# Kernel optimization log

Measured on AMD Instinct MI355X. Metric: run time of the kernel, lower is better.

## Reference

```python
import jax, jax.numpy as jnp
import numpy as np
import math

B, D = 8192, 128
STEEPNESS = 1.0
TOPK_NEG = 10
N_SORT = TOPK_NEG + 1  # n_pos_augs - 1 + topk_neg = 1 + 10
EPS = 1e-8


def setup_inputs() -> dict:
    key = jax.random.key(0)
    k1, k2 = jax.random.split(key)
    aug1 = jax.random.normal(k1, (B, D), dtype=jnp.float32)
    aug2 = jax.random.normal(k2, (B, D), dtype=jnp.float32)
    return {"aug1": aug1, "aug2": aug2}


def _soft_sort_odd_even(x, steepness):
    """Differentiable odd-even transposition sort (diffsort, cauchy interpolation).
    x: [B, n]. Returns (sorted_x [B, n], P [B, n, n]) where sorted_x = x @ P and
    P[i, j] = relaxed probability that input element i lands at sorted position j."""
    b, n = x.shape
    P = jnp.broadcast_to(jnp.eye(n, dtype=x.dtype), (b, n, n))
    for layer in range(n):  # n layers, alternating even/odd pairs
        off = layer % 2
        idx_a = np.arange(off, n - 1, 2)
        idx_b = idx_a + 1
        a = x[:, idx_a]
        bb = x[:, idx_b]
        # cauchy CDF relaxation: alpha -> 1 when b > a (already ordered)
        alpha = jnp.arctan(steepness * (bb - a)) / math.pi + 0.5
        x = x.at[:, idx_a].set(alpha * a + (1.0 - alpha) * bb)
        x = x.at[:, idx_b].set((1.0 - alpha) * a + alpha * bb)
        Pa = P[:, :, idx_a]
        Pb = P[:, :, idx_b]
        al = alpha[:, None, :]
        P = P.at[:, :, idx_a].set(al * Pa + (1.0 - al) * Pb)
        P = P.at[:, :, idx_b].set((1.0 - al) * Pa + al * Pb)
    return x, P


def _bce(p, t):
    # torch.nn.BCELoss with log clamped at -100
    logp = jnp.clip(jnp.log(p), -100.0, None)
    log1mp = jnp.clip(jnp.log(1.0 - p), -100.0, None)
    return -jnp.mean(t * logp + (1.0 - t) * log1mp)


def _compute_loss(anchor, positive):
    anchor = anchor.astype(jnp.float32)
    positive = jax.lax.stop_gradient(positive.astype(jnp.float32))  # stop_grad=True
    # pairwise cosine similarity (dim=1)
    an = anchor / jnp.maximum(jnp.linalg.norm(anchor, axis=1, keepdims=True), EPS)
    pn = positive / jnp.maximum(jnp.linalg.norm(positive, axis=1, keepdims=True), EPS)
    pos_sims = jnp.sum(an * pn, axis=1, keepdims=True)  # [B, 1]; sort over dim=1 is a no-op
    # all-to-all cosine similarity vs detached anchors (negatives = anchor.detach())
    negs = jax.lax.stop_gradient(an)
    sim = an @ negs.T  # [B, B]
    nb = sim.shape[0]
    sim = jnp.where(jnp.eye(nb, dtype=bool), -jnp.inf, sim)  # mask self-similarity
    neg_top, _ = jax.lax.top_k(sim, TOPK_NEG)  # descending
    neg_top = neg_top[:, ::-1]                 # flip -> ascending
    sims = jnp.concatenate([neg_top, pos_sims], axis=1)  # [B, 11]
    _, P = _soft_sort_odd_even(sims, STEEPNESS)
    n = sims.shape[1]
    # perm_target = identity -> column-sum targets are first-k indicators
    p_neg = jnp.clip(jnp.sum(P[:, :, :TOPK_NEG], axis=2), 0.0, 1.0)  # [B, n]
    p_pos = jnp.clip(jnp.sum(P[:, :, TOPK_NEG:], axis=2), 0.0, 1.0)
    t_neg = jnp.broadcast_to((jnp.arange(n) < TOPK_NEG).astype(jnp.float32), (nb, n))
    t_pos = 1.0 - t_neg
    return 0.5 * (_bce(p_pos, t_pos) + _bce(p_neg, t_neg))


def reference(aug1, aug2):
    # n_augs = 2: each aug serves as anchor once, the other as the single positive
    loss1 = _compute_loss(aug1, aug2)
    loss2 = _compute_loss(aug2, aug1)
    return (loss1 + loss2) / 2.0
```

## Files before the change

kernel.cpp:

```cpp
#include <hip/hip_runtime.h>
#include <cstdint>
#include <cmath>

#define NB 8192
#define ND 128
#define CAP 64
#define NEG_INF (-__builtin_inff())

typedef __attribute__((ext_vector_type(8))) __bf16 bf16x8;
typedef __attribute__((ext_vector_type(2))) __bf16 bf16x2;
typedef __attribute__((ext_vector_type(4))) float f32x4;


__device__ __forceinline__ void insert10(float t[10], float v) {
#pragma unroll
  for (int j = 0; j < 9; ++j) t[j] = __builtin_amdgcn_fmed3f(t[j], t[j + 1], v);
  t[9] = fmaxf(t[9], v);
}
__device__ __forceinline__ void insert11(float t[11], float v) {
#pragma unroll
  for (int j = 0; j < 10; ++j) t[j] = __builtin_amdgcn_fmed3f(t[j], t[j + 1], v);
  t[10] = fmaxf(t[10], v);
}

__device__ float row_loss(float x[11]) {
  float al[55];
#pragma unroll
  for (int layer = 0; layer < 11; ++layer) {
#pragma unroll
    for (int p = 0; p < 5; ++p) {
      int ii = (layer & 1) + 2 * p;
      float av = x[ii], bv = x[ii + 1];
      float a = atanf(bv - av) * 0.3183098861837907f + 0.5f;
      al[layer * 5 + p] = a;
      float be = 1.f - a;
      x[ii] = a * av + be * bv;
      x[ii + 1] = be * av + a * bv;
    }
  }
  float v[11];
#pragma unroll
  for (int i = 0; i < 11; ++i) v[i] = 0.f;
  v[10] = 1.f;
#pragma unroll
  for (int layer = 10; layer >= 0; --layer) {
#pragma unroll
    for (int p = 0; p < 5; ++p) {
      int ii = (layer & 1) + 2 * p;
      float a = al[layer * 5 + p];
      float be = 1.f - a;
      float va = v[ii], vb = v[ii + 1];
      v[ii] = a * va + be * vb;
      v[ii + 1] = be * va + a * vb;
    }
  }
  float C = fmaxf(logf(v[10]), -100.f);
#pragma unroll
  for (int i = 0; i < 10; ++i) C += fmaxf(logf(1.f - v[i]), -100.f);
  return C;
}

__global__ __launch_bounds__(256, 4) void knorm(const float* __restrict__ aug1,
                                                const float* __restrict__ aug2,
                                                __bf16* __restrict__ an,
                                                float* __restrict__ pos,
                                                float* __restrict__ out) {
  if (blockIdx.x == 0 && threadIdx.x == 0) out[0] = 0.f;
  int wid = threadIdx.x >> 6;
  int l = threadIdx.x & 63;
  int row = blockIdx.x * 4 + wid;
  const float2* a1 = (const float2*)(aug1) + (size_t)row * 64;
  const float2* a2 = (const float2*)(aug2) + (size_t)row * 64;
  float2 v1 = a1[l], v2 = a2[l];
  float ss1 = v1.x * v1.x + v1.y * v1.y;
  float ss2 = v2.x * v2.x + v2.y * v2.y;
  float dp = v1.x * v2.x + v1.y * v2.y;
#pragma unroll
  for (int off = 1; off < 64; off <<= 1) {
    ss1 += __shfl_xor(ss1, off);
    ss2 += __shfl_xor(ss2, off);
    dp += __shfl_xor(dp, off);
  }
  float inv1 = 1.0f / fmaxf(sqrtf(ss1), 1e-8f);
  float inv2 = 1.0f / fmaxf(sqrtf(ss2), 1e-8f);
  bf16x2 o1, o2;
  o1[0] = (__bf16)(v1.x * inv1);
  o1[1] = (__bf16)(v1.y * inv1);
  o2[0] = (__bf16)(v2.x * inv2);
  o2[1] = (__bf16)(v2.y * inv2);
  int unit = ((row >> 4) << 8) + ((l >> 4) << 6) + (((l >> 2) & 3) << 4) + (row & 15);
  ((bf16x2*)(an))[unit * 4 + (l & 3)] = o1;
  ((bf16x2*)(an + (size_t)NB * ND))[unit * 4 + (l & 3)] = o2;
  if (l == 0) pos[row] = dp * inv1 * inv2;
}

__device__ __forceinline__ void consume4(const f32x4* acc, float (*cand)[CAP],
                                         int* lcnt, float tau, int c) {
#pragma unroll
  for (int rb = 0; rb < 4; ++rb) {
    int rl = rb * 16 + c;
#pragma unroll
    for (int r = 0; r < 4; ++r) {
      float v = acc[rb][r];
      if (v > tau) {
        int s = atomicAdd(&lcnt[rl], 1);
        if (s < CAP) cand[rl][s] = v;
      }
    }
  }
}

__global__ __launch_bounds__(256, 3) void kgram(const __bf16* __restrict__ an_all,
                                                float* __restrict__ tk,
                                                int* __restrict__ cnth,
                                                float* __restrict__ taug) {
  int dir = blockIdx.y;
  int rowg = blockIdx.x >> 1;
  int half = blockIdx.x & 1;
  const bf16x8* an8 = (const bf16x8*)(an_all + (size_t)dir * NB * ND);
  int w = threadIdx.x >> 6;
  int l = threadIdx.x & 63;
  int q = l >> 4;
  int c = l & 15;
  int row_base = rowg * 64;
  const int col0 = half * 4096;

  __shared__ float cand[64][CAP];
  __shared__ int lcnt[64];
  __shared__ float sred[2][4];
  if (threadIdx.x < 64) lcnt[threadIdx.x] = 0;

  bf16x8 brow[4][4];
#pragma unroll
  for (int rb = 0; rb < 4; ++rb)
#pragma unroll
    for (int kc = 0; kc < 4; ++kc)
      brow[rb][kc] = an8[(size_t)row_base * 16 + rb * 256 + kc * 64 + l];

  const bf16x8* pf0 = an8 + ((size_t)col0 * 16 + w * 256 + l);
  bf16x8 a[4], a2[4];
  const f32x4 zz = {0.f, 0.f, 0.f, 0.f};
  f32x4 accA[4], accB[4];

  auto loadA = [&](int t) {
    const bf16x8* p = pf0 + (size_t)(t & 63) * 1024;
#pragma unroll
    for (int kc = 0; kc < 4; ++kc) a[kc] = p[kc * 64];
  };
  auto loadA2 = [&](int t) {
    const bf16x8* p = pf0 + (size_t)(t & 63) * 1024;
#pragma unroll
    for (int kc = 0; kc < 4; ++kc) a2[kc] = p[kc * 64];
  };
  auto mfma_tile = [&](f32x4* A, const bf16x8* src) {
#pragma unroll
    for (int rb = 0; rb < 4; ++rb)
      A[rb] = __builtin_amdgcn_mfma_f32_16x16x32_bf16(src[0], brow[rb][0], zz, 0, 0, 0);
#pragma unroll
    for (int kc = 1; kc < 4; ++kc)
#pragma unroll
      for (int rb = 0; rb < 4; ++rb)
        A[rb] = __builtin_amdgcn_mfma_f32_16x16x32_bf16(src[kc], brow[rb][kc], A[rb], 0, 0, 0);
  };

  loadA(0);
  mfma_tile(accA, a);
  loadA2(1);
  bool diag0 = (row_base == col0);
  int cq0 = col0 + w * 16 + q * 4;
  float s1 = 0.f, s2 = 0.f;
#pragma unroll
  for (int rb = 0; rb < 4; ++rb) {
    int myrow = row_base + rb * 16 + c;
#pragma unroll
    for (int r = 0; r < 4; ++r) {
      float v = accA[rb][r];
      v = (diag0 && (cq0 + r == myrow)) ? 0.f : v;
      s1 += v;
      s2 = fmaf(v, v, s2);
    }
  }
#pragma unroll
  for (int off = 1; off < 64; off <<= 1) {
    s1 += __shfl_xor(s1, off);
    s2 += __shfl_xor(s2, off);
  }
  if (l == 0) { sred[0][w] = s1; sred[1][w] = s2; }
  __syncthreads();
  float n = diag0 ? 4032.f : 4096.f;
  float ts1 = sred[0][0] + sred[0][1] + sred[0][2] + sred[0][3];
  float ts2 = sred[1][0] + sred[1][1] + sred[1][2] + sred[1][3];
  float mu = ts1 / n;
  float sig = sqrtf(fmaxf(ts2 / n - mu * mu, 0.f));
  float tau = mu + 2.5f * sig;
  if (threadIdx.x == 0) taug[(dir * 128 + rowg) * 2 + half] = tau;
  consume4(accA, cand, lcnt, tau, c);

  mfma_tile(accA, a2);
  loadA(2);
  for (int t = 2; t < 64; t += 2) {
    mfma_tile(accB, a);
    loadA2(t + 1);
    consume4(accA, cand, lcnt, tau, c);
    mfma_tile(accA, a2);
    loadA(t + 2);
    consume4(accB, cand, lcnt, tau, c);
  }
  consume4(accA, cand, lcnt, tau, c);

  __syncthreads();
  if (threadIdx.x < 64) {
    int rl = threadIdx.x;
    int cc = lcnt[rl];
    float t11[11];
#pragma unroll
    for (int j = 0; j < 11; ++j) t11[j] = NEG_INF;
    int m = cc < CAP ? cc : CAP;
    for (int i = 0; i < m; ++i) {
      float v = cand[rl][i];
      if (v > t11[0]) insert11(t11, v);
    }
    bool diagq = (row_base >= col0) && (row_base < col0 + 4096);
    float* o = tk + ((size_t)(dir * NB + row_base + rl) * 2 + half) * 10;
    if (diagq) {
#pragma unroll
      for (int j = 0; j < 10; ++j) o[j] = t11[j];
    } else {
#pragma unroll
      for (int j = 0; j < 10; ++j) o[j] = t11[j + 1];
    }
    cnth[(dir * NB + row_base + rl) * 2 + half] = cc;
  }
}

__global__ __launch_bounds__(64, 1) void ksort(const float* __restrict__ tk,
                                               const float* __restrict__ pos,
                                               const int* __restrict__ cnth,
                                               const float* __restrict__ taug,
                                               const __bf16* __restrict__ an_all,
                                               float* __restrict__ out) {
  int tid = blockIdx.x * 64 + threadIdx.x;
  int dir = tid >> 13;
  int row = tid & (NB - 1);
  int lane = threadIdx.x;

  const float* A = tk + (size_t)(dir * NB + row) * 20;
  float s10[10];
#pragma unroll
  for (int j = 0; j < 10; ++j) s10[j] = A[j];
#pragma unroll
  for (int j = 0; j < 10; ++j) {
    float v = A[10 + j];
    if (v > s10[0]) insert10(s10, v);
  }
  int rowg = row >> 6;
  float tmax = fmaxf(taug[(dir * 128 + rowg) * 2], taug[(dir * 128 + rowg) * 2 + 1]);
  int2 cc2 = ((const int2*)cnth)[dir * NB + row];
  bool ok = (cc2.x <= CAP) && (cc2.y <= CAP) && (s10[0] >= tmax);

  float C = 0.f;
  if (ok) {
    float x[11];
#pragma unroll
    for (int j = 0; j < 10; ++j) x[j] = s10[j];
    x[10] = pos[row];
    C = row_loss(x);
  }
#pragma unroll
  for (int off = 1; off < 64; off <<= 1) C += __shfl_xor(C, off);
  if (lane == 0) atomicAdd(out, C * (-1.f / (2.f * (float)NB * 11.f)));

  unsigned long long bad = __ballot(!ok);
  if (bad == 0ull) return;
  __shared__ float rv[128];
  __shared__ float lst[64][10];
  const __bf16* an = an_all + (size_t)dir * NB * ND;
  const bf16x8* an8 = (const bf16x8*)an;
  while (bad) {
    int b = __ffsll((long long)bad) - 1;
    bad &= bad - 1;
    int brow = (blockIdx.x * 64 + b) & (NB - 1);
    int u = ((brow >> 4) << 8) + ((lane >> 4) << 6) + (((lane >> 2) & 3) << 4) + (brow & 15);
    bf16x2 pr = ((const bf16x2*)an)[u * 4 + (lane & 3)];
    rv[lane * 2] = (float)pr[0];
    rv[lane * 2 + 1] = (float)pr[1];
    __syncthreads();
    float t10[10];
#pragma unroll
    for (int j = 0; j < 10; ++j) t10[j] = NEG_INF;
    for (int i = 0; i < 128; ++i) {
      int col = lane + i * 64;
      if (col == brow) continue;
      float d = 0.f;
#pragma unroll
      for (int j = 0; j < 16; ++j) {
        bf16x8 p = an8[(size_t)(col >> 4) * 256 + (j >> 2) * 64 + (j & 3) * 16 + (col & 15)];
        int kb = (j >> 2) * 32 + (j & 3) * 8;
#pragma unroll
        for (int e = 0; e < 8; ++e) d = fmaf(rv[kb + e], (float)p[e], d);
      }
      if (d > t10[0]) insert10(t10, d);
    }
#pragma unroll
    for (int j = 0; j < 10; ++j) lst[lane][j] = t10[j];
    __syncthreads();
    if (lane == 0) {
      float cur[10];
#pragma unroll
      for (int j = 0; j < 10; ++j) cur[j] = lst[0][j];
      for (int s = 1; s < 64; ++s)
        for (int j = 0; j < 10; ++j) {
          float v = lst[s][j];
          if (v > cur[0]) insert10(cur, v);
        }
      float x[11];
#pragma unroll
      for (int j = 0; j < 10; ++j) x[j] = cur[j];
      x[10] = pos[brow];
      atomicAdd(out, row_loss(x) * (-1.f / (2.f * (float)NB * 11.f)));
    }
    __syncthreads();
  }
}

extern "C" void kernel_launch(void* const* d_in, const int* in_sizes, int n_in,
                              void* d_out, int out_size, void* d_ws, size_t ws_size,
                              hipStream_t stream) {
  const float* aug1 = (const float*)d_in[0];
  const float* aug2 = (const float*)d_in[1];
  char* w = (char*)d_ws;
  __bf16* an = (__bf16*)w;
  float* pos = (float*)(w + (size_t)4 * 1024 * 1024);
  float* tk = pos + NB;
  int* cnth = (int*)(tk + (size_t)2 * NB * 20);
  float* taug = (float*)(cnth + 2 * NB * 2);

  knorm<<<dim3(NB / 4), dim3(256), 0, stream>>>(aug1, aug2, an, pos, (float*)d_out);
  kgram<<<dim3(256, 2), dim3(256), 0, stream>>>(an, tk, cnth, taug);
  ksort<<<dim3(2 * NB / 64), dim3(64), 0, stream>>>(tk, pos, cnth, taug, an, (float*)d_out);
}
```

Baseline: 129.9 us.

## Enlarge gram row tile to 128 and split columns into quarters

Each gram block now keeps 128 anchor rows in registers and scans a quarter of the columns, where before it kept 64 rows and scanned half. Each loaded column tile feeds twice as many MFMAs, so column traffic per output drops, and the top-k merge in ksort now combines four partial lists. The candidate buffer shrinks to 48 entries with a padded stride of 49 to cut shared-memory bank conflicts, and MFMA sections raise wave priority with s_setprio. In exchange, register pressure roughly doubles (occupancy bound drops from 3 to 2 blocks), the per-quarter threshold is estimated from a different sample, and the smaller cap may push more rows onto the fallback path.

```diff
diff --git a/kernel.cpp b/kernel.cpp
--- a/kernel.cpp
+++ b/kernel.cpp
@@ -4,7 +4,8 @@
 
 #define NB 8192
 #define ND 128
-#define CAP 64
+#define CAP 48
+#define CAPP 49
 #define NEG_INF (-__builtin_inff())
 
 typedef __attribute__((ext_vector_type(8))) __bf16 bf16x8;
@@ -94,45 +95,29 @@
   if (l == 0) pos[row] = dp * inv1 * inv2;
 }
 
-__device__ __forceinline__ void consume4(const f32x4* acc, float (*cand)[CAP],
-                                         int* lcnt, float tau, int c) {
-#pragma unroll
-  for (int rb = 0; rb < 4; ++rb) {
-    int rl = rb * 16 + c;
-#pragma unroll
-    for (int r = 0; r < 4; ++r) {
-      float v = acc[rb][r];
-      if (v > tau) {
-        int s = atomicAdd(&lcnt[rl], 1);
-        if (s < CAP) cand[rl][s] = v;
-      }
-    }
-  }
-}
-
-__global__ __launch_bounds__(256, 3) void kgram(const __bf16* __restrict__ an_all,
+__global__ __launch_bounds__(256, 2) void kgram(const __bf16* __restrict__ an_all,
                                                 float* __restrict__ tk,
                                                 int* __restrict__ cnth,
                                                 float* __restrict__ taug) {
   int dir = blockIdx.y;
-  int rowg = blockIdx.x >> 1;
-  int half = blockIdx.x & 1;
+  int rowg = blockIdx.x >> 2;
+  int quar = blockIdx.x & 3;
   const bf16x8* an8 = (const bf16x8*)(an_all + (size_t)dir * NB * ND);
   int w = threadIdx.x >> 6;
   int l = threadIdx.x & 63;
   int q = l >> 4;
   int c = l & 15;
-  int row_base = rowg * 64;
-  const int col0 = half * 4096;
-
-  __shared__ float cand[64][CAP];
-  __shared__ int lcnt[64];
+  int row_base = rowg * 128;
+  const int col0 = quar * 2048;
+
+  __shared__ float cand[128][CAPP];
+  __shared__ int lcnt[128];
   __shared__ float sred[2][4];
-  if (threadIdx.x < 64) lcnt[threadIdx.x] = 0;
-
-  bf16x8 brow[4][4];
-#pragma unroll
-  for (int rb = 0; rb < 4; ++rb)
+  if (threadIdx.x < 128) lcnt[threadIdx.x] = 0;
+
+  bf16x8 brow[8][4];
+#pragma unroll
+  for (int rb = 0; rb < 8; ++rb)
 #pragma unroll
     for (int kc = 0; kc < 4; ++kc)
       brow[rb][kc] = an8[(size_t)row_base * 16 + rb * 256 + kc * 64 + l];
@@ -140,42 +125,56 @@
   const bf16x8* pf0 = an8 + ((size_t)col0 * 16 + w * 256 + l);
   bf16x8 a[4], a2[4];
   const f32x4 zz = {0.f, 0.f, 0.f, 0.f};
-  f32x4 accA[4], accB[4];
+  f32x4 accA[8], accB[8];
 
   auto loadA = [&](int t) {
-    const bf16x8* p = pf0 + (size_t)(t & 63) * 1024;
+    const bf16x8* p = pf0 + (size_t)(t & 31) * 1024;
 #pragma unroll
     for (int kc = 0; kc < 4; ++kc) a[kc] = p[kc * 64];
   };
   auto loadA2 = [&](int t) {
-    const bf16x8* p = pf0 + (size_t)(t & 63) * 1024;
+    const bf16x8* p = pf0 + (size_t)(t & 31) * 1024;
 #pragma unroll
     for (int kc = 0; kc < 4; ++kc) a2[kc] = p[kc * 64];
   };
   auto mfma_tile = [&](f32x4* A, const bf16x8* src) {
-#pragma unroll
-    for (int rb = 0; rb < 4; ++rb)
+    __builtin_amdgcn_s_setprio(1);
+#pragma unroll
+    for (int rb = 0; rb < 8; ++rb)
       A[rb] = __builtin_amdgcn_mfma_f32_16x16x32_bf16(src[0], brow[rb][0], zz, 0, 0, 0);
 #pragma unroll
     for (int kc = 1; kc < 4; ++kc)
 #pragma unroll
-      for (int rb = 0; rb < 4; ++rb)
+      for (int rb = 0; rb < 8; ++rb)
         A[rb] = __builtin_amdgcn_mfma_f32_16x16x32_bf16(src[kc], brow[rb][kc], A[rb], 0, 0, 0);
+    __builtin_amdgcn_s_setprio(0);
+  };
+  auto consume = [&](const f32x4* acc, float tau) {
+#pragma unroll
+    for (int rb = 0; rb < 8; ++rb) {
+      int rl = rb * 16 + c;
+#pragma unroll
+      for (int r = 0; r < 4; ++r) {
+        float v = acc[rb][r];
+        if (v > tau) {
+          int s = atomicAdd(&lcnt[rl], 1);
+          if (s < CAP) cand[rl][s] = v;
+        }
+      }
+    }
   };
 
   loadA(0);
   mfma_tile(accA, a);
   loadA2(1);
   bool diag0 = (row_base == col0);
-  int cq0 = col0 + w * 16 + q * 4;
   float s1 = 0.f, s2 = 0.f;
 #pragma unroll
-  for (int rb = 0; rb < 4; ++rb) {
-    int myrow = row_base + rb * 16 + c;
+  for (int rb = 0; rb < 8; ++rb) {
 #pragma unroll
     for (int r = 0; r < 4; ++r) {
       float v = accA[rb][r];
-      v = (diag0 && (cq0 + r == myrow)) ? 0.f : v;
+      v = (diag0 && (w * 16 + q * 4 + r == rb * 16 + c)) ? 0.f : v;
       s1 += v;
       s2 = fmaf(v, v, s2);
     }
@@ -187,29 +186,29 @@
   }
   if (l == 0) { sred[0][w] = s1; sred[1][w] = s2; }
   __syncthreads();
-  float n = diag0 ? 4032.f : 4096.f;
+  float n = diag0 ? 8128.f : 8192.f;
   float ts1 = sred[0][0] + sred[0][1] + sred[0][2] + sred[0][3];
   float ts2 = sred[1][0] + sred[1][1] + sred[1][2] + sred[1][3];
   float mu = ts1 / n;
   float sig = sqrtf(fmaxf(ts2 / n - mu * mu, 0.f));
   float tau = mu + 2.5f * sig;
-  if (threadIdx.x == 0) taug[(dir * 128 + rowg) * 2 + half] = tau;
-  consume4(accA, cand, lcnt, tau, c);
+  if (threadIdx.x == 0) taug[((size_t)dir * 64 + rowg) * 4 + quar] = tau;
+  consume(accA, tau);
 
   mfma_tile(accA, a2);
   loadA(2);
-  for (int t = 2; t < 64; t += 2) {
+  for (int t = 2; t < 32; t += 2) {
     mfma_tile(accB, a);
     loadA2(t + 1);
-    consume4(accA, cand, lcnt, tau, c);
+    consume(accA, tau);
     mfma_tile(accA, a2);
     loadA(t + 2);
-    consume4(accB, cand, lcnt, tau, c);
-  }
-  consume4(accA, cand, lcnt, tau, c);
+    consume(accB, tau);
+  }
+  consume(accA, tau);
 
   __syncthreads();
-  if (threadIdx.x < 64) {
+  if (threadIdx.x < 128) {
     int rl = threadIdx.x;
     int cc = lcnt[rl];
     float t11[11];
@@ -220,8 +219,9 @@
       float v = cand[rl][i];
       if (v > t11[0]) insert11(t11, v);
     }
-    bool diagq = (row_base >= col0) && (row_base < col0 + 4096);
-    float* o = tk + ((size_t)(dir * NB + row_base + rl) * 2 + half) * 10;
+    bool diagq = ((rowg >> 4) == quar);
+    int row = row_base + rl;
+    float* o = tk + ((size_t)(dir * NB + row) * 4 + quar) * 10;
     if (diagq) {
 #pragma unroll
       for (int j = 0; j < 10; ++j) o[j] = t11[j];
@@ -229,7 +229,7 @@
 #pragma unroll
       for (int j = 0; j < 10; ++j) o[j] = t11[j + 1];
     }
-    cnth[(dir * NB + row_base + rl) * 2 + half] = cc;
+    cnth[(size_t)(dir * NB + row) * 4 + quar] = cc;
   }
 }
 
@@ -244,19 +244,24 @@
   int row = tid & (NB - 1);
   int lane = threadIdx.x;
 
-  const float* A = tk + (size_t)(dir * NB + row) * 20;
+  const float* A = tk + (size_t)(dir * NB + row) * 40;
   float s10[10];
 #pragma unroll
   for (int j = 0; j < 10; ++j) s10[j] = A[j];
 #pragma unroll
-  for (int j = 0; j < 10; ++j) {
-    float v = A[10 + j];
-    if (v > s10[0]) insert10(s10, v);
-  }
-  int rowg = row >> 6;
-  float tmax = fmaxf(taug[(dir * 128 + rowg) * 2], taug[(dir * 128 + rowg) * 2 + 1]);
-  int2 cc2 = ((const int2*)cnth)[dir * NB + row];
-  bool ok = (cc2.x <= CAP) && (cc2.y <= CAP) && (s10[0] >= tmax);
+  for (int h = 1; h < 4; ++h) {
+#pragma unroll
+    for (int j = 0; j < 10; ++j) {
+      float v = A[h * 10 + j];
+      if (v > s10[0]) insert10(s10, v);
+    }
+  }
+  int rowg = row >> 7;
+  const float* tg = taug + ((size_t)dir * 64 + rowg) * 4;
+  float tmax = fmaxf(fmaxf(tg[0], tg[1]), fmaxf(tg[2], tg[3]));
+  int4 cc4 = ((const int4*)cnth)[dir * NB + row];
+  bool ok = (cc4.x <= CAP) && (cc4.y <= CAP) && (cc4.z <= CAP) &&
+            (cc4.w <= CAP) && (s10[0] >= tmax);
 
   float C = 0.f;
   if (ok) {
@@ -332,8 +337,8 @@
   __bf16* an = (__bf16*)w;
   float* pos = (float*)(w + (size_t)4 * 1024 * 1024);
   float* tk = pos + NB;
-  int* cnth = (int*)(tk + (size_t)2 * NB * 20);
-  float* taug = (float*)(cnth + 2 * NB * 2);
+  int* cnth = (int*)(tk + (size_t)2 * NB * 40);
+  float* taug = (float*)(cnth + (size_t)2 * NB * 4);
 
   knorm<<<dim3(NB / 4), dim3(256), 0, stream>>>(aug1, aug2, an, pos, (float*)d_out);
   kgram<<<dim3(256, 2), dim3(256), 0, stream>>>(an, tk, cnth, taug);
```

After: 130.8 us. Within noise of the previous version (+0.7%).
